# Kernel tuning notes

Hardware: AMD Instinct MI355X
Metric: run time of the kernel (lower is better)

Reference implementation:

```python
import jax, jax.numpy as jnp
import numpy as np

HEADS = 16
DIM_HEAD = 64
BLOCK = 16
SEQ_LEN = 2048
NUM_BLOCKS = SEQ_LEN // BLOCK  # 128
NUM_RANDOM_BLOCKS = 32
LOCAL_WINDOW = 4
GLOBAL_BLOCKS = [0]


def make_layout():
    # Deterministic stand-in for DeepSpeed VariableSparsityConfig.make_layout
    # (local windows of 4 blocks + random blocks + global block columns/rows,
    #  then tril for unidirectional attention).
    rng = np.random.RandomState(0)
    nb = NUM_BLOCKS
    layout = np.zeros((nb, nb), dtype=bool)
    for w in range(0, nb, LOCAL_WINDOW):
        layout[w:w + LOCAL_WINDOW, w:w + LOCAL_WINDOW] = True
    rnd = rng.randint(0, nb, size=(nb, NUM_RANDOM_BLOCKS))
    layout[np.arange(nb)[:, None], rnd] = True
    for g in GLOBAL_BLOCKS:
        layout[:, g] = True
        layout[g, :] = True
    layout = np.tril(layout)  # unidirectional
    return jnp.asarray(layout)


def setup_inputs() -> dict:
    key = jax.random.key(0)
    k1, k2, k3 = jax.random.split(key, 3)
    dim = 1024
    inner = HEADS * DIM_HEAD  # 1024
    x = jax.random.normal(k1, (2, SEQ_LEN, dim), dtype=jnp.float32)
    w_qkv = jax.random.normal(k2, (dim, 3 * inner), dtype=jnp.float32) * 0.02
    w_out = jax.random.normal(k3, (inner, dim), dtype=jnp.float32) * 0.02
    b_out = jnp.zeros((dim,), dtype=jnp.float32)
    layout = make_layout()  # [128, 128] bool
    return {"x": x, "w_qkv": w_qkv, "w_out": w_out, "b_out": b_out, "layout": layout}


def reference(x, w_qkv, w_out, b_out, layout):
    b, n, _ = x.shape
    scale = DIM_HEAD ** -0.5
    qkv = x @ w_qkv  # [b, n, 3*h*d]
    q, k, v = jnp.split(qkv, 3, axis=-1)
    split_heads = lambda t: t.reshape(b, n, HEADS, DIM_HEAD).transpose(0, 2, 1, 3)
    q, k, v = split_heads(q), split_heads(k), split_heads(v)  # [b, h, n, d]

    scores = jnp.einsum('bhid,bhjd->bhij', q, k) * scale  # [b, h, n, n]
    neg = -jnp.finfo(scores.dtype).max
    # additive causal attn_mask (value = -finfo.max / 2, attn_mask_mode='add')
    causal = jnp.triu(jnp.ones((n, n), dtype=bool), 1)
    scores = scores + jnp.where(causal, neg / 2, jnp.zeros((), scores.dtype))
    # block-sparse layout: entries outside allowed blocks are fully masked
    allowed = jnp.repeat(jnp.repeat(layout, BLOCK, axis=0), BLOCK, axis=1)  # [n, n]
    scores = jnp.where(allowed, scores, neg)
    attn = jax.nn.softmax(scores, axis=-1)
    out = jnp.einsum('bhij,bhjd->bhid', attn, v)  # [b, h, n, d]
    out = out.transpose(0, 2, 1, 3).reshape(b, n, HEADS * DIM_HEAD)
    return out @ w_out + b_out
```

## Files before the change

### kernel.cpp

```cpp
#include <hip/hip_runtime.h>
#include <cstdint>
#include <cstddef>


typedef short bf8 __attribute__((ext_vector_type(8)));
typedef float f32x4 __attribute__((ext_vector_type(4)));
typedef unsigned short u16;
typedef unsigned int u32;

#define MFMA_BF16(a, b, c) __builtin_amdgcn_mfma_f32_16x16x32_bf16((a), (b), (c), 0, 0, 0)

constexpr int SEQ = 2048;
constexpr int NH = 16;
constexpr int DHD = 64;
constexpr int NBLK = 128;
constexpr int DIM = 1024;

__device__ __forceinline__ u32 pack2bf(float a, float b) {
  u32 r;
  asm("v_cvt_pk_bf16_f32 %0, %1, %2" : "=v"(r) : "v"(a), "v"(b));
  return r;
}
__device__ __forceinline__ void gload_lds16(const u16* g, u16* l) {
  auto gp = (const __attribute__((address_space(1))) u16*)(g);
  auto lp = (__attribute__((address_space(3))) u16*)(l);
  __builtin_amdgcn_global_load_lds(gp, lp, 16, 0, 0);
}

__global__ __launch_bounds__(256) void prep(
    const float* __restrict__ x, u16* __restrict__ xbf,
    const float* __restrict__ wqkv, u16* __restrict__ wqkvT,
    const float* __restrict__ wout, u16* __restrict__ woutT,
    const unsigned char* __restrict__ lay,
    int* __restrict__ cnt, int* __restrict__ cols) {
  __shared__ u16 tile[64][72];
  int bid = blockIdx.x;
  int t = threadIdx.x;

  if (bid < 2048) {
    int idx = (bid * 256 + t) * 8;
    float4 a = *(const float4*)(x + idx);
    float4 b = *(const float4*)(x + idx + 4);
    *(uint4*)(xbf + idx) = make_uint4(pack2bf(a.x, a.y), pack2bf(a.z, a.w),
                                      pack2bf(b.x, b.y), pack2bf(b.z, b.w));
    return;
  }
  bid -= 2048;
  if (bid < 768 + 256) {
    const float* in; u16* out; int C, bx, by;
    if (bid < 768) { in = wqkv; out = wqkvT; C = 3072; bx = bid % 48; by = bid / 48; }
    else { int r = bid - 768; in = wout; out = woutT; C = 1024; bx = r % 16; by = r / 16; }
    const int R = 1024;
    int c0 = bx * 64, r0 = by * 64;
    int rr = t >> 4, cc = (t & 15) * 4;
    #pragma unroll
    for (int p = 0; p < 64; p += 16) {
      float4 v = *(const float4*)(in + (size_t)(r0 + rr + p) * C + c0 + cc);
      *(u32*)&tile[rr + p][cc + 0] = pack2bf(v.x, v.y);
      *(u32*)&tile[rr + p][cc + 2] = pack2bf(v.z, v.w);
    }
    __syncthreads();
    int oc = t >> 3, orr = (t & 7) * 8;
    #pragma unroll
    for (int p = 0; p < 64; p += 32) {
      u16 tmp[8];
      #pragma unroll
      for (int qy = 0; qy < 8; qy++) tmp[qy] = tile[orr + qy][oc + p];
      u16* dst = out + (size_t)(c0 + oc + p) * R + r0 + orr;
      *(ushort4*)(dst)     = make_ushort4(tmp[0], tmp[1], tmp[2], tmp[3]);
      *(ushort4*)(dst + 4) = make_ushort4(tmp[4], tmp[5], tmp[6], tmp[7]);
    }
    return;
  }
  bid -= 1024;
  int wave = t >> 6, lane = t & 63;
  int i = bid * 4 + wave;
  const uint4* l4 = (const uint4*)lay;
  u32 acc = 0;
  #pragma unroll
  for (int it = 0; it < 16; it++) {
    uint4 v = l4[it * 64 + lane];
    acc |= ((v.x | v.y | v.z | v.w) & 0xFFFFFF00u);
  }
  bool as_int32 = (__ballot(acc != 0) == 0ULL);
  const int* li = (const int*)lay;
  int j0 = lane, j1 = lane + 64;
  bool p0 = (j0 <= i) && (as_int32 ? (li[i * 128 + j0] != 0) : (lay[i * 128 + j0] != 0));
  bool p1 = (j1 <= i) && (as_int32 ? (li[i * 128 + j1] != 0) : (lay[i * 128 + j1] != 0));
  unsigned long long m0 = __ballot(p0), m1 = __ballot(p1);
  unsigned long long lt = (1ULL << lane) - 1ULL;
  int base0 = __popcll(m0);
  if (p0) cols[i * 128 + __popcll(m0 & lt)] = j0;
  if (p1) cols[i * 128 + base0 + __popcll(m1 & lt)] = j1;
  if (lane == 0) cnt[i] = base0 + __popcll(m1);
}

__global__ __launch_bounds__(256) void gemm_qkv(
    const u16* __restrict__ A, const u16* __restrict__ Bt,
    u16* __restrict__ oq, u16* __restrict__ okk, u16* __restrict__ ov) {
  __shared__ u16 smem[16896];
  u16* bA0 = smem;
  u16* bB0 = smem + 4096;
  u16* bA1 = smem + 8192;
  u16* bB1 = smem + 12288;
  const int K = 1024;
  int tid = threadIdx.x, lane = tid & 63, wave = tid >> 6;
  int quad = lane >> 4, l16 = lane & 15;
  int wr = wave >> 1, wc = wave & 1;
  int d = blockIdx.x;
  int xcd = d & 7, rest = d >> 3;
  int bm = xcd + (rest & 3) * 8;
  int bn = rest >> 2;
  int bm0 = bm * 128, bn0 = bn * 128;

  f32x4 acc[4][4];
  #pragma unroll
  for (int i = 0; i < 4; i++)
    #pragma unroll
    for (int j = 0; j < 4; j++) acc[i][j] = (f32x4){0.f, 0.f, 0.f, 0.f};

  int srow = lane >> 2;
  int schunk = ((lane & 3) ^ (srow & 3)) * 8;
  int phys = (quad ^ (l16 & 3)) * 8;

  auto stage = [&](u16* dA, u16* dB, int k0) {
    #pragma unroll
    for (int r = 0; r < 2; r++) {
      int row = wave * 32 + r * 16;
      gload_lds16(A  + (size_t)(bm0 + row + srow) * K + k0 + schunk, dA + row * 32);
      gload_lds16(Bt + (size_t)(bn0 + row + srow) * K + k0 + schunk, dB + row * 32);
    }
  };
  auto compute = [&](const u16* cA, const u16* cB) {
    bf8 af[4], bfr[4];
    #pragma unroll
    for (int i = 0; i < 4; i++)
      af[i] = *(const bf8*)(cA + (wr * 64 + i * 16 + l16) * 32 + phys);
    #pragma unroll
    for (int j = 0; j < 4; j++)
      bfr[j] = *(const bf8*)(cB + (wc * 64 + j * 16 + l16) * 32 + phys);
    #pragma unroll
    for (int i = 0; i < 4; i++)
      #pragma unroll
      for (int j = 0; j < 4; j++)
        acc[i][j] = MFMA_BF16(af[i], bfr[j], acc[i][j]);
  };

  stage(bA0, bB0, 0);
  for (int k0 = 0; k0 < K; k0 += 64) {
    __syncthreads();
    if (k0 + 32 < K) stage(bA1, bB1, k0 + 32);
    compute(bA0, bB0);
    __syncthreads();
    if (k0 + 64 < K) stage(bA0, bB0, k0 + 64);
    compute(bA1, bB1);
  }

  int which = bn0 >> 10;
  if (which == 2) {
    #pragma unroll
    for (int j = 0; j < 4; j++) {
      int c = bn0 + wc * 64 + j * 16 + l16;
      int h = (c & 1023) >> 6, dd = c & 63;
      #pragma unroll
      for (int i = 0; i < 4; i++) {
        int r0 = bm0 + wr * 64 + i * 16;
        int b = r0 >> 11, nn0 = r0 & 2047, jb = nn0 >> 4;
        u16* dst = ov + ((size_t)((b * NH + h) * NBLK + jb) * DHD + dd) * 16 + quad * 4;
        *(uint2*)dst = make_uint2(pack2bf(acc[i][j][0], acc[i][j][1]),
                                  pack2bf(acc[i][j][2], acc[i][j][3]));
      }
    }
  } else {
    u16* dstbase = (which == 0) ? oq : okk;
    float m = (which == 0) ? 0.18033688f : 1.0f;
    __syncthreads();
    #pragma unroll
    for (int j = 0; j < 4; j++) {
      int col = wc * 64 + j * 16 + l16;
      #pragma unroll
      for (int i = 0; i < 4; i++) {
        int row = wr * 64 + i * 16 + quad * 4;
        *(uint2*)&smem[col * 132 + row] =
            make_uint2(pack2bf(acc[i][j][0] * m, acc[i][j][1] * m),
                       pack2bf(acc[i][j][2] * m, acc[i][j][3] * m));
      }
    }
    __syncthreads();
    int r = tid >> 1, half = tid & 1;
    int rglob = bm0 + r;
    int b = rglob >> 11, nn = rglob & 2047;
    int h = ((bn0 & 1023) >> 6) + half;
    #pragma unroll
    for (int j = 0; j < 4; j++) {
      union { u16 t[16]; uint4 q[2]; } tv;
      #pragma unroll
      for (int dd = 0; dd < 16; dd++)
        tv.t[dd] = smem[(half * 64 + j * 16 + dd) * 132 + r];
      u16* dst = dstbase + ((size_t)(b * NH + h) * SEQ + nn) * DHD + j * 16;
      *(uint4*)(dst) = tv.q[0];
      *(uint4*)(dst + 8) = tv.q[1];
    }
  }
}

__global__ __launch_bounds__(256) void gemm_out(
    const u16* __restrict__ A, const u16* __restrict__ Bt,
    float* __restrict__ of, const float* __restrict__ bias) {
  __shared__ u16 smem[12288];
  u16* bA0 = smem;
  u16* bB0 = smem + 4096;
  u16* bA1 = smem + 6144;
  u16* bB1 = smem + 10240;
  const int K = 1024, N = 1024;
  int tid = threadIdx.x, lane = tid & 63, wave = tid >> 6;
  int quad = lane >> 4, l16 = lane & 15;
  int wr = wave >> 1, wc = wave & 1;
  int d = blockIdx.x;
  int xcd = d & 7, slot = d >> 3;
  int bm = xcd * 4 + (slot & 3);
  int bn = slot >> 2;
  int bm0 = bm * 128, bn0 = bn * 64;

  f32x4 acc[4][2];
  #pragma unroll
  for (int i = 0; i < 4; i++)
    #pragma unroll
    for (int j = 0; j < 2; j++) acc[i][j] = (f32x4){0.f, 0.f, 0.f, 0.f};

  int srow = lane >> 2;
  int schunk = ((lane & 3) ^ (srow & 3)) * 8;
  int phys = (quad ^ (l16 & 3)) * 8;

  auto stage = [&](u16* dA, u16* dB, int k0) {
    #pragma unroll
    for (int r = 0; r < 2; r++) {
      int row = wave * 32 + r * 16;
      gload_lds16(A + (size_t)(bm0 + row + srow) * K + k0 + schunk, dA + row * 32);
    }
    int brow = wave * 16;
    gload_lds16(Bt + (size_t)(bn0 + brow + srow) * K + k0 + schunk, dB + brow * 32);
  };
  auto compute = [&](const u16* cA, const u16* cB) {
    bf8 af[4], bfr[2];
    #pragma unroll
    for (int i = 0; i < 4; i++)
      af[i] = *(const bf8*)(cA + (wr * 64 + i * 16 + l16) * 32 + phys);
    #pragma unroll
    for (int j = 0; j < 2; j++)
      bfr[j] = *(const bf8*)(cB + (wc * 32 + j * 16 + l16) * 32 + phys);
    #pragma unroll
    for (int i = 0; i < 4; i++)
      #pragma unroll
      for (int j = 0; j < 2; j++)
        acc[i][j] = MFMA_BF16(af[i], bfr[j], acc[i][j]);
  };

  stage(bA0, bB0, 0);
  for (int k0 = 0; k0 < K; k0 += 64) {
    __syncthreads();
    if (k0 + 32 < K) stage(bA1, bB1, k0 + 32);
    compute(bA0, bB0);
    __syncthreads();
    if (k0 + 64 < K) stage(bA0, bB0, k0 + 64);
    compute(bA1, bB1);
  }

  #pragma unroll
  for (int j = 0; j < 2; j++) {
    int c = bn0 + wc * 32 + j * 16 + l16;
    float bv = bias[c];
    #pragma unroll
    for (int i = 0; i < 4; i++) {
      int rbase = bm0 + wr * 64 + i * 16 + quad * 4;
      #pragma unroll
      for (int ii = 0; ii < 4; ii++)
        of[(size_t)(rbase + ii) * N + c] = acc[i][j][ii] + bv;
    }
  }
}

__global__ __launch_bounds__(256) void attn_sparse(
    const u16* __restrict__ q, const u16* __restrict__ k, const u16* __restrict__ vblk,
    const int* __restrict__ cnt, const int* __restrict__ cols,
    u16* __restrict__ aout) {
  __shared__ u32 pbuf[4][320];
  int wave = threadIdx.x >> 6, lane = threadIdx.x & 63;
  int quad = lane >> 4, l16 = lane & 15;
  int blk = blockIdx.x;
  int xcd = blk & 7, rest = blk >> 3;
  int bh = xcd * 4 + (rest & 3);
  int strip = rest >> 2;
  int qb = 127 - (strip * 4 + wave);
  u32* pbw = pbuf[wave];

  const u16* qp = q + ((size_t)bh * SEQ + qb * 16) * DHD + l16 * DHD + quad * 8;
  bf8 qa0 = *(const bf8*)(qp);
  bf8 qa1 = *(const bf8*)(qp + 32);

  float l_i = 0.f;
  f32x4 o[4];
  #pragma unroll
  for (int t = 0; t < 4; t++) o[t] = (f32x4){0.f, 0.f, 0.f, 0.f};

  int count = cnt[qb];
  const int* mc = cols + qb * NBLK;

  bf8 bufA[8], bufB[8];
  int ja0 = 0, ja1 = 0, jb0b = 0, jb1b = 0;
  bool hvA = false, hvB = false;

  auto ldpair = [&](int p, bf8* kv, int& o0, int& o1, bool& ohv) {
    o0 = mc[p];
    ohv = (p + 1 < count);
    o1 = ohv ? mc[p + 1] : o0;
    const u16* kp0 = k + ((size_t)bh * SEQ + o0 * 16) * DHD + l16 * DHD + quad * 8;
    kv[0] = *(const bf8*)(kp0); kv[1] = *(const bf8*)(kp0 + 32);
    const u16* kp1 = k + ((size_t)bh * SEQ + o1 * 16) * DHD + l16 * DHD + quad * 8;
    kv[2] = *(const bf8*)(kp1); kv[3] = *(const bf8*)(kp1 + 32);
    int jq = (quad < 2) ? o0 : o1;
    const u16* vp = vblk + (size_t)(bh * NBLK + jq) * 1024 + l16 * 16 + (quad & 1) * 8;
    kv[4] = *(const bf8*)(vp);
    kv[5] = *(const bf8*)(vp + 256);
    kv[6] = *(const bf8*)(vp + 512);
    kv[7] = *(const bf8*)(vp + 768);
  };

  ldpair(0, bufA, ja0, ja1, hvA);
  if (2 < count) ldpair(2, bufB, jb0b, jb1b, hvB);

  for (int p = 0; p < count; p += 2) {
    __builtin_amdgcn_s_setprio(1);
    f32x4 S0 = (f32x4){0.f, 0.f, 0.f, 0.f};
    S0 = MFMA_BF16(bufA[0], qa0, S0);
    S0 = MFMA_BF16(bufA[1], qa1, S0);
    f32x4 S1 = (f32x4){0.f, 0.f, 0.f, 0.f};
    S1 = MFMA_BF16(bufA[2], qa0, S1);
    S1 = MFMA_BF16(bufA[3], qa1, S1);
    __builtin_amdgcn_s_setprio(0);

    float e0[4], e1[4];
    #pragma unroll
    for (int r = 0; r < 4; r++) {
      int kl = quad * 4 + r;
      float s0 = S0[r];
      if (ja0 == qb && kl > l16) s0 = -1e38f;
      float s1 = hvA ? S1[r] : -1e38f;
      if (hvA && ja1 == qb && kl > l16) s1 = -1e38f;
      e0[r] = exp2f(s0);
      e1[r] = exp2f(s1);
      l_i += e0[r] + e1[r];
    }

    *(uint2*)(&pbw[l16 * 20 + quad * 2]) =
        make_uint2(pack2bf(e0[0], e0[1]), pack2bf(e0[2], e0[3]));
    *(uint2*)(&pbw[l16 * 20 + 8 + quad * 2]) =
        make_uint2(pack2bf(e1[0], e1[1]), pack2bf(e1[2], e1[3]));
    union { uint4 w; bf8 v; } pf;
    pf.w = *(const uint4*)(&pbw[l16 * 20 + quad * 4]);

    __builtin_amdgcn_s_setprio(1);
    o[0] = MFMA_BF16(bufA[4], pf.v, o[0]);
    o[1] = MFMA_BF16(bufA[5], pf.v, o[1]);
    o[2] = MFMA_BF16(bufA[6], pf.v, o[2]);
    o[3] = MFMA_BF16(bufA[7], pf.v, o[3]);
    __builtin_amdgcn_s_setprio(0);

    #pragma unroll
    for (int z = 0; z < 8; z++) bufA[z] = bufB[z];
    ja0 = jb0b; ja1 = jb1b; hvA = hvB;
    if (p + 4 < count) ldpair(p + 4, bufB, jb0b, jb1b, hvB);
  }

  float l = l_i;
  l += __shfl_xor(l, 16);
  l += __shfl_xor(l, 32);
  float inv = 1.0f / l;
  int b = bh >> 4, h = bh & 15;
  int n = qb * 16 + l16;
  u16* dst = aout + ((size_t)b * SEQ + n) * DIM + h * DHD;
  #pragma unroll
  for (int t = 0; t < 4; t++) {
    *(uint2*)(dst + t * 16 + quad * 4) =
        make_uint2(pack2bf(o[t][0] * inv, o[t][1] * inv),
                   pack2bf(o[t][2] * inv, o[t][3] * inv));
  }
}

extern "C" void kernel_launch(void* const* d_in, const int* in_sizes, int n_in,
                              void* d_out, int out_size, void* d_ws, size_t ws_size,
                              hipStream_t stream) {
  const float* x      = (const float*)d_in[0];
  const float* w_qkv  = (const float*)d_in[1];
  const float* w_out  = (const float*)d_in[2];
  const float* b_out  = (const float*)d_in[3];
  const unsigned char* layout = (const unsigned char*)d_in[4];
  float* out = (float*)d_out;

  char* ws = (char*)d_ws;
  u16* xbf   = (u16*)(ws);
  u16* wqkvT = (u16*)(ws + (8u  << 20));
  u16* woutT = (u16*)(ws + (14u << 20) + (512u << 10));
  u16* qB    = (u16*)(ws + (17u << 20));
  u16* kB    = (u16*)(ws + (25u << 20));
  u16* vblk  = (u16*)(ws + (33u << 20));
  u16* aout  = (u16*)(ws + (41u << 20));
  int* cnt   = (int*)(ws + (49u << 20));
  int* cols  = (int*)(ws + (49u << 20) + 4096);

  prep<<<3104, 256, 0, stream>>>(x, xbf, w_qkv, wqkvT, w_out, woutT,
                                 layout, cnt, cols);
  gemm_qkv<<<768, 256, 0, stream>>>(xbf, wqkvT, qB, kB, vblk);
  attn_sparse<<<1024, 256, 0, stream>>>(qB, kB, vblk, cnt, cols, aout);
  gemm_out<<<512, 256, 0, stream>>>(aout, woutT, out, b_out);
}
```

Before: 165.2 us.

## Replace LDS P transpose with permlane swaps and unroll double-buffer loop

The per-wave shared-memory round trip used to reshape the softmax probabilities into the MFMA B-operand layout is replaced by v_permlane32_swap and v_permlane16_swap register exchanges, removing LDS writes and reads plus their wait latency. The main loop is also unrolled by two so each iteration alternates between the A and B register buffers instead of copying bufB into bufA. This drops eight bf8 register moves per step but relies on the permlane lane mapping matching the old LDS layout exactly.

```diff
diff --git a/kernel.cpp b/kernel.cpp
--- a/kernel.cpp
+++ b/kernel.cpp
@@ -284,7 +284,6 @@
     const u16* __restrict__ q, const u16* __restrict__ k, const u16* __restrict__ vblk,
     const int* __restrict__ cnt, const int* __restrict__ cols,
     u16* __restrict__ aout) {
-  __shared__ u32 pbuf[4][320];
   int wave = threadIdx.x >> 6, lane = threadIdx.x & 63;
   int quad = lane >> 4, l16 = lane & 15;
   int blk = blockIdx.x;
@@ -292,7 +291,6 @@
   int bh = xcd * 4 + (rest & 3);
   int strip = rest >> 2;
   int qb = 127 - (strip * 4 + wave);
-  u32* pbw = pbuf[wave];
 
   const u16* qp = q + ((size_t)bh * SEQ + qb * 16) * DHD + l16 * DHD + quad * 8;
   bf8 qa0 = *(const bf8*)(qp);
@@ -307,8 +305,8 @@
   const int* mc = cols + qb * NBLK;
 
   bf8 bufA[8], bufB[8];
-  int ja0 = 0, ja1 = 0, jb0b = 0, jb1b = 0;
-  bool hvA = false, hvB = false;
+  int jA0 = 0, jA1 = 0, jB0 = 0, jB1 = 0;
+  bool hA = false, hB = false;
 
   auto ldpair = [&](int p, bf8* kv, int& o0, int& o1, bool& ohv) {
     o0 = mc[p];
@@ -326,17 +324,14 @@
     kv[7] = *(const bf8*)(vp + 768);
   };
 
-  ldpair(0, bufA, ja0, ja1, hvA);
-  if (2 < count) ldpair(2, bufB, jb0b, jb1b, hvB);
-
-  for (int p = 0; p < count; p += 2) {
+  auto process = [&](const bf8* buf, int j0, int j1, bool hv) {
     __builtin_amdgcn_s_setprio(1);
     f32x4 S0 = (f32x4){0.f, 0.f, 0.f, 0.f};
-    S0 = MFMA_BF16(bufA[0], qa0, S0);
-    S0 = MFMA_BF16(bufA[1], qa1, S0);
+    S0 = MFMA_BF16(buf[0], qa0, S0);
+    S0 = MFMA_BF16(buf[1], qa1, S0);
     f32x4 S1 = (f32x4){0.f, 0.f, 0.f, 0.f};
-    S1 = MFMA_BF16(bufA[2], qa0, S1);
-    S1 = MFMA_BF16(bufA[3], qa1, S1);
+    S1 = MFMA_BF16(buf[2], qa0, S1);
+    S1 = MFMA_BF16(buf[3], qa1, S1);
     __builtin_amdgcn_s_setprio(0);
 
     float e0[4], e1[4];
@@ -344,32 +339,41 @@
     for (int r = 0; r < 4; r++) {
       int kl = quad * 4 + r;
       float s0 = S0[r];
-      if (ja0 == qb && kl > l16) s0 = -1e38f;
-      float s1 = hvA ? S1[r] : -1e38f;
-      if (hvA && ja1 == qb && kl > l16) s1 = -1e38f;
+      if (j0 == qb && kl > l16) s0 = -1e38f;
+      float s1 = hv ? S1[r] : -1e38f;
+      if (hv && j1 == qb && kl > l16) s1 = -1e38f;
       e0[r] = exp2f(s0);
       e1[r] = exp2f(s1);
       l_i += e0[r] + e1[r];
     }
 
-    *(uint2*)(&pbw[l16 * 20 + quad * 2]) =
-        make_uint2(pack2bf(e0[0], e0[1]), pack2bf(e0[2], e0[3]));
-    *(uint2*)(&pbw[l16 * 20 + 8 + quad * 2]) =
-        make_uint2(pack2bf(e1[0], e1[1]), pack2bf(e1[2], e1[3]));
+    u32 a0 = pack2bf(e0[0], e0[1]);
+    u32 a1 = pack2bf(e0[2], e0[3]);
+    u32 a2 = pack2bf(e1[0], e1[1]);
+    u32 a3 = pack2bf(e1[2], e1[3]);
+    asm("v_permlane32_swap_b32 %0, %1" : "+v"(a0), "+v"(a2));
+    asm("v_permlane32_swap_b32 %0, %1" : "+v"(a1), "+v"(a3));
+    asm("v_permlane16_swap_b32 %0, %1" : "+v"(a0), "+v"(a2));
+    asm("v_permlane16_swap_b32 %0, %1" : "+v"(a1), "+v"(a3));
     union { uint4 w; bf8 v; } pf;
-    pf.w = *(const uint4*)(&pbw[l16 * 20 + quad * 4]);
+    pf.w = make_uint4(a0, a1, a2, a3);
 
     __builtin_amdgcn_s_setprio(1);
-    o[0] = MFMA_BF16(bufA[4], pf.v, o[0]);
-    o[1] = MFMA_BF16(bufA[5], pf.v, o[1]);
-    o[2] = MFMA_BF16(bufA[6], pf.v, o[2]);
-    o[3] = MFMA_BF16(bufA[7], pf.v, o[3]);
+    o[0] = MFMA_BF16(buf[4], pf.v, o[0]);
+    o[1] = MFMA_BF16(buf[5], pf.v, o[1]);
+    o[2] = MFMA_BF16(buf[6], pf.v, o[2]);
+    o[3] = MFMA_BF16(buf[7], pf.v, o[3]);
     __builtin_amdgcn_s_setprio(0);
-
-    #pragma unroll
-    for (int z = 0; z < 8; z++) bufA[z] = bufB[z];
-    ja0 = jb0b; ja1 = jb1b; hvA = hvB;
-    if (p + 4 < count) ldpair(p + 4, bufB, jb0b, jb1b, hvB);
+  };
+
+  ldpair(0, bufA, jA0, jA1, hA);
+  if (2 < count) ldpair(2, bufB, jB0, jB1, hB);
+
+  for (int p = 0; p < count; p += 4) {
+    process(bufA, jA0, jA1, hA);
+    if (p + 4 < count) ldpair(p + 4, bufA, jA0, jA1, hA);
+    if (p + 2 < count) process(bufB, jB0, jB1, hB);
+    if (p + 6 < count) ldpair(p + 6, bufB, jB0, jB1, hB);
   }
 
   float l = l_i;
```

New measurement: 169.3 us. 1.02x slower.
